# Kernel tuning notes

Hardware: AMD Instinct MI355X
Metric: run time of the kernel (lower is better)

## Reference

```python
import jax, jax.numpy as jnp
import numpy as np

N_NODES = 50000
N_EDGES = 800000
D = 128
N_REL = 4
N_GRAPHS = 128
N_CLASSES = 16


def rgcn_layer(x, W_rel, W_root, b, src, dst, edge_type):
    # Per-relation transform of all nodes: [N, R, D]
    xt = jnp.einsum('nd,rdf->nrf', x, W_rel)
    msg = xt[src, edge_type]  # [E, D] gather message per edge
    # mean aggregation per (dst, relation) pair (PyG RGCNConv aggr='mean')
    seg = dst * N_REL + edge_type
    cnt = jax.ops.segment_sum(jnp.ones((src.shape[0],), x.dtype), seg,
                              num_segments=N_NODES * N_REL)
    norm = 1.0 / jnp.maximum(cnt[seg], 1.0)
    agg = jax.ops.segment_sum(msg * norm[:, None], dst, num_segments=N_NODES)
    return agg + x @ W_root + b


def setup_inputs() -> dict:
    key = jax.random.key(0)
    ks = jax.random.split(key, 12)
    s = 1.0 / np.sqrt(D)
    inp = {
        'x': jax.random.normal(ks[0], (N_NODES, D), jnp.float32),
        'edge_index': jax.random.randint(ks[1], (2, N_EDGES), 0, N_NODES, jnp.int64),
        'edge_type': jax.random.randint(ks[2], (N_EDGES,), 0, N_REL, jnp.int64),
        'batch': jnp.sort(jax.random.randint(ks[3], (N_NODES,), 0, N_GRAPHS, jnp.int64)),
        'W_rel1': jax.random.normal(ks[4], (N_REL, D, D), jnp.float32) * s,
        'W_root1': jax.random.normal(ks[5], (D, D), jnp.float32) * s,
        'b1': jnp.zeros((D,), jnp.float32),
        'W_rel2': jax.random.normal(ks[6], (N_REL, D, D), jnp.float32) * s,
        'W_root2': jax.random.normal(ks[7], (D, D), jnp.float32) * s,
        'b2': jnp.zeros((D,), jnp.float32),
        'W_cls': jax.random.normal(ks[8], (D, N_CLASSES), jnp.float32) * s,
        'b_cls': jnp.zeros((N_CLASSES,), jnp.float32),
    }
    return inp


def reference(x, edge_index, edge_type, batch, W_rel1, W_root1, b1,
              W_rel2, W_root2, b2, W_cls, b_cls):
    src, dst = edge_index[0], edge_index[1]
    h = jax.nn.relu(rgcn_layer(x, W_rel1, W_root1, b1, src, dst, edge_type))
    h = jax.nn.relu(rgcn_layer(h, W_rel2, W_root2, b2, src, dst, edge_type))
    # global mean pool over graphs (dropout is identity: training=False)
    gsum = jax.ops.segment_sum(h, batch, num_segments=N_GRAPHS)
    gcnt = jax.ops.segment_sum(jnp.ones((h.shape[0],), h.dtype), batch,
                               num_segments=N_GRAPHS)
    g = gsum / jnp.maximum(gcnt, 1.0)[:, None]
    return g @ W_cls + b_cls
```

## Files before the change

kernel.cpp:

```cpp
#include <hip/hip_runtime.h>

#define D_DIM 128
#define N_REL 4
#define CAP 32

typedef __attribute__((ext_vector_type(8))) short bf16x8;
typedef __attribute__((ext_vector_type(4))) float f32x4;

static inline int cdiv(int a, int b) { return (a + b - 1) / b; }

__device__ inline ushort f2bf(float f) {
    union { float f; unsigned u; } v;
    v.f = f;
    unsigned r = v.u + 0x7FFFu + ((v.u >> 16) & 1u);
    return (ushort)(r >> 16);
}

__device__ inline float bf2f(ushort u) {
    union { unsigned u; float f; } v;
    v.u = (unsigned)u << 16;
    return v.f;
}

__device__ inline float uif(unsigned u) {
    union { unsigned u; float f; } v;
    v.u = u;
    return v.f;
}

#define CNT_B 391
#define CAST_B 782
#define CAST_FULL 781
#define PACK_B 80

__global__ __launch_bounds__(256) void prep_kernel(
    const float* __restrict__ x, ushort* __restrict__ Xb,
    const int* __restrict__ src, const int* __restrict__ dst,
    const int* __restrict__ et, unsigned* __restrict__ icnt,
    ushort* __restrict__ esorted,
    const float* __restrict__ Wrel1, const float* __restrict__ Wroot1,
    const float* __restrict__ Wrel2, const float* __restrict__ Wroot2,
    ushort* __restrict__ Wpk1, ushort* __restrict__ Wpk2,
    int n4, int nEdges) {
    int b = blockIdx.x;
    if (b < CNT_B) {
        int e = (b * 256 + threadIdx.x) * 8;
        if (e >= nEdges) return;
        if (e + 8 <= nEdges) {
            int4 sA = *(const int4*)(src + e);
            int4 sB = *(const int4*)(src + e + 4);
            int4 dA = *(const int4*)(dst + e);
            int4 dB = *(const int4*)(dst + e + 4);
            int4 tA = *(const int4*)(et + e);
            int4 tB = *(const int4*)(et + e + 4);
            unsigned o0 = atomicAdd(&icnt[dA.x], 1u << (8 * tA.x));
            unsigned o1 = atomicAdd(&icnt[dA.y], 1u << (8 * tA.y));
            unsigned o2 = atomicAdd(&icnt[dA.z], 1u << (8 * tA.z));
            unsigned o3 = atomicAdd(&icnt[dA.w], 1u << (8 * tA.w));
            unsigned o4 = atomicAdd(&icnt[dB.x], 1u << (8 * tB.x));
            unsigned o5 = atomicAdd(&icnt[dB.y], 1u << (8 * tB.y));
            unsigned o6 = atomicAdd(&icnt[dB.z], 1u << (8 * tB.z));
            unsigned o7 = atomicAdd(&icnt[dB.w], 1u << (8 * tB.w));
            int r0 = (int)(((o0 >> (8 * tA.x)) & 0xFFu) - 0xAAu);
            int r1 = (int)(((o1 >> (8 * tA.y)) & 0xFFu) - 0xAAu);
            int r2 = (int)(((o2 >> (8 * tA.z)) & 0xFFu) - 0xAAu);
            int r3 = (int)(((o3 >> (8 * tA.w)) & 0xFFu) - 0xAAu);
            int r4 = (int)(((o4 >> (8 * tB.x)) & 0xFFu) - 0xAAu);
            int r5 = (int)(((o5 >> (8 * tB.y)) & 0xFFu) - 0xAAu);
            int r6 = (int)(((o6 >> (8 * tB.z)) & 0xFFu) - 0xAAu);
            int r7 = (int)(((o7 >> (8 * tB.w)) & 0xFFu) - 0xAAu);
            esorted[((size_t)(dA.x * N_REL + tA.x) << 5) + r0] = (ushort)sA.x;
            esorted[((size_t)(dA.y * N_REL + tA.y) << 5) + r1] = (ushort)sA.y;
            esorted[((size_t)(dA.z * N_REL + tA.z) << 5) + r2] = (ushort)sA.z;
            esorted[((size_t)(dA.w * N_REL + tA.w) << 5) + r3] = (ushort)sA.w;
            esorted[((size_t)(dB.x * N_REL + tB.x) << 5) + r4] = (ushort)sB.x;
            esorted[((size_t)(dB.y * N_REL + tB.y) << 5) + r5] = (ushort)sB.y;
            esorted[((size_t)(dB.z * N_REL + tB.z) << 5) + r6] = (ushort)sB.z;
            esorted[((size_t)(dB.w * N_REL + tB.w) << 5) + r7] = (ushort)sB.w;
        } else {
            for (int j = 0; e + j < nEdges; ++j) {
                int dd = dst[e + j], tt = et[e + j];
                unsigned o = atomicAdd(&icnt[dd], 1u << (8 * tt));
                int r = (int)(((o >> (8 * tt)) & 0xFFu) - 0xAAu);
                esorted[((size_t)(dd * N_REL + tt) << 5) + r] = (ushort)src[e + j];
            }
        }
    } else if (b < CNT_B + CAST_B) {
        int rb = b - CNT_B;
        int base = rb * 2048 + threadIdx.x;
        if (rb < CAST_FULL) {
            float4 v0 = ((const float4*)x)[base];
            float4 v1 = ((const float4*)x)[base + 256];
            float4 v2 = ((const float4*)x)[base + 512];
            float4 v3 = ((const float4*)x)[base + 768];
            float4 v4 = ((const float4*)x)[base + 1024];
            float4 v5 = ((const float4*)x)[base + 1280];
            float4 v6 = ((const float4*)x)[base + 1536];
            float4 v7 = ((const float4*)x)[base + 1792];
            ushort4 o0, o1, o2, o3, o4, o5, o6, o7;
            o0.x = f2bf(v0.x); o0.y = f2bf(v0.y); o0.z = f2bf(v0.z); o0.w = f2bf(v0.w);
            o1.x = f2bf(v1.x); o1.y = f2bf(v1.y); o1.z = f2bf(v1.z); o1.w = f2bf(v1.w);
            o2.x = f2bf(v2.x); o2.y = f2bf(v2.y); o2.z = f2bf(v2.z); o2.w = f2bf(v2.w);
            o3.x = f2bf(v3.x); o3.y = f2bf(v3.y); o3.z = f2bf(v3.z); o3.w = f2bf(v3.w);
            o4.x = f2bf(v4.x); o4.y = f2bf(v4.y); o4.z = f2bf(v4.z); o4.w = f2bf(v4.w);
            o5.x = f2bf(v5.x); o5.y = f2bf(v5.y); o5.z = f2bf(v5.z); o5.w = f2bf(v5.w);
            o6.x = f2bf(v6.x); o6.y = f2bf(v6.y); o6.z = f2bf(v6.z); o6.w = f2bf(v6.w);
            o7.x = f2bf(v7.x); o7.y = f2bf(v7.y); o7.z = f2bf(v7.z); o7.w = f2bf(v7.w);
            ((ushort4*)Xb)[base] = o0;
            ((ushort4*)Xb)[base + 256] = o1;
            ((ushort4*)Xb)[base + 512] = o2;
            ((ushort4*)Xb)[base + 768] = o3;
            ((ushort4*)Xb)[base + 1024] = o4;
            ((ushort4*)Xb)[base + 1280] = o5;
            ((ushort4*)Xb)[base + 1536] = o6;
            ((ushort4*)Xb)[base + 1792] = o7;
        } else {
#pragma unroll
            for (int j = 0; j < 8; ++j) {
                int i = base + j * 256;
                if (i < n4) {
                    float4 v = ((const float4*)x)[i];
                    ushort4 o;
                    o.x = f2bf(v.x); o.y = f2bf(v.y); o.z = f2bf(v.z); o.w = f2bf(v.w);
                    ((ushort4*)Xb)[i] = o;
                }
            }
        }
    } else {
        int pb = b - (CNT_B + CAST_B);
        int layer = pb / 40;
        int rem = pb % 40;
        int mat = rem >> 3;
        int blk = rem & 7;
        const float* Wrel = layer ? Wrel2 : Wrel1;
        const float* Wroot = layer ? Wroot2 : Wroot1;
        ushort* out = layer ? Wpk2 : Wpk1;
        const float* W = (mat < N_REL) ? (Wrel + (size_t)mat * D_DIM * D_DIM) : Wroot;
        int t = blk * 256 + threadIdx.x;
        int lane = t & 63;
        int tile = t >> 6;
        int kt = tile >> 3;
        int nt = tile & 7;
        int n = nt * 16 + (lane & 15);
        int kb = kt * 32 + (lane >> 4) * 8;
        ushort* o = out + (((size_t)mat * 32 + tile) * 64 + lane) * 8;
        ushort4 lo, hi;
        lo.x = f2bf(W[(kb + 0) * D_DIM + n]);
        lo.y = f2bf(W[(kb + 1) * D_DIM + n]);
        lo.z = f2bf(W[(kb + 2) * D_DIM + n]);
        lo.w = f2bf(W[(kb + 3) * D_DIM + n]);
        hi.x = f2bf(W[(kb + 4) * D_DIM + n]);
        hi.y = f2bf(W[(kb + 5) * D_DIM + n]);
        hi.z = f2bf(W[(kb + 6) * D_DIM + n]);
        hi.w = f2bf(W[(kb + 7) * D_DIM + n]);
        *(ushort4*)(o) = lo;
        *(ushort4*)(o + 4) = hi;
    }
}

template <bool DO_SORT>
__global__ __launch_bounds__(256, DO_SORT ? 7 : 8) void layer_kernel(
    const ushort* __restrict__ Xb, const unsigned* __restrict__ icnt,
    ushort* __restrict__ esorted, const ushort* __restrict__ Wpk,
    const float* __restrict__ bias, ushort* __restrict__ outb, int n_nodes) {
    __shared__ ushort Ms[16][520];
    __shared__ ushort sid16[DO_SORT ? 16 : 1][4][34];
    const int tid = threadIdx.x;
    const int wave = tid >> 6;
    const int lane = tid & 63;
    const int ql = tid & 15;
    const int qd = tid >> 4;
    const int m = lane & 15;
    const int q = lane >> 4;
    const int r0 = blockIdx.x * 16;
    const int rel = qd & 3;
    const int rowgrp = qd >> 2;
    const int lanebase = (qd & 3) * 16;

    unsigned cw4[4], idw[4];
#pragma unroll
    for (int p = 0; p < 4; ++p) {
        int node = r0 + p * 4 + rowgrp;
        int vnode = min(node, n_nodes - 1);
        cw4[p] = (node < n_nodes) ? icnt[vnode] : 0xAAAAAAAAu;
        idw[p] = ((const unsigned*)(esorted +
                  (((size_t)vnode * N_REL + rel) << 5)))[ql];
    }

    if constexpr (DO_SORT) {
#pragma unroll
        for (int p = 0; p < 4; ++p) {
            const int deg = (int)(((cw4[p] >> (rel * 8)) & 0xFFu) - 0xAAu);
            if (deg >= 1) {
                const int j0 = 2 * ql, j1 = 2 * ql + 1;
                const int v0 = (int)(idw[p] & 0xFFFFu);
                const int v1 = (int)(idw[p] >> 16);
                int rk0 = 0, rk1 = 0;
                const int nw = (deg + 1) >> 1;
                for (int kk = 0; kk < nw; ++kk) {
                    unsigned w = (unsigned)__shfl((int)idw[p], lanebase + kk, 64);
                    int k0 = 2 * kk, k1 = 2 * kk + 1;
                    int wlo = (int)(w & 0xFFFFu), whi = (int)(w >> 16);
                    rk0 += (wlo < v0 || (wlo == v0 && k0 < j0)) ? 1 : 0;
                    rk1 += (wlo < v1 || (wlo == v1 && k0 < j1)) ? 1 : 0;
                    if (k1 < deg) {
                        rk0 += (whi < v0 || (whi == v0 && k1 < j0)) ? 1 : 0;
                        rk1 += (whi < v1 || (whi == v1 && k1 < j1)) ? 1 : 0;
                    }
                }
                if (j0 < deg) sid16[qd][p][rk0] = (ushort)v0;
                if (j1 < deg) sid16[qd][p][rk1] = (ushort)v1;
            }
        }
        __threadfence_block();
#pragma unroll
        for (int p = 0; p < 4; ++p) {
            const int deg = (int)(((cw4[p] >> (rel * 8)) & 0xFFu) - 0xAAu);
            if (deg >= 2 && 2 * ql < deg) {
                int node = r0 + p * 4 + rowgrp;
                unsigned* rowp = (unsigned*)(esorted +
                                 (((size_t)node * N_REL + rel) << 5));
                rowp[ql] = (unsigned)sid16[qd][p][2 * ql] |
                           ((unsigned)sid16[qd][p][2 * ql + 1] << 16);
            }
        }
        __threadfence_block();
    }

    auto acc8 = [](float* a, uint4 u) {
        a[0] += uif(u.x << 16); a[1] += uif(u.x & 0xFFFF0000u);
        a[2] += uif(u.y << 16); a[3] += uif(u.y & 0xFFFF0000u);
        a[4] += uif(u.z << 16); a[5] += uif(u.z & 0xFFFF0000u);
        a[6] += uif(u.w << 16); a[7] += uif(u.w & 0xFFFF0000u);
    };

    const ushort* xb = Xb + ql * 8;
#pragma unroll
    for (int p = 0; p < 4; ++p) {
        const int row = p * 4 + rowgrp;
        const int deg = (int)(((cw4[p] >> (rel * 8)) & 0xFFu) - 0xAAu);
        uint4* mrow = (uint4*)&Ms[row][rel * 128 + ql * 8];
        if (deg <= 0) {
            *mrow = make_uint4(0u, 0u, 0u, 0u);
            continue;
        }
        auto getid = [&](int e) -> size_t {
            if constexpr (DO_SORT) {
                return (size_t)sid16[qd][p][e] * D_DIM;
            } else {
                unsigned w = (unsigned)__shfl((int)idw[p], lanebase + (e >> 1), 64);
                return (size_t)((e & 1) ? (w >> 16) : (w & 0xFFFFu)) * D_DIM;
            }
        };
        float a[8], b[8];
#pragma unroll
        for (int j = 0; j < 8; ++j) { a[j] = 0.f; b[j] = 0.f; }
        int e = 0;
        for (; e + 4 <= deg; e += 4) {
            size_t s0 = getid(e);
            size_t s1 = getid(e + 1);
            size_t s2 = getid(e + 2);
            size_t s3 = getid(e + 3);
            uint4 u0 = *(const uint4*)(xb + s0);
            uint4 u1 = *(const uint4*)(xb + s1);
            uint4 u2 = *(const uint4*)(xb + s2);
            uint4 u3 = *(const uint4*)(xb + s3);
            acc8(a, u0); acc8(b, u1); acc8(a, u2); acc8(b, u3);
        }
        if (e + 2 <= deg) {
            size_t s0 = getid(e);
            size_t s1 = getid(e + 1);
            uint4 u0 = *(const uint4*)(xb + s0);
            uint4 u1 = *(const uint4*)(xb + s1);
            acc8(a, u0); acc8(b, u1);
            e += 2;
        }
        if (e < deg) {
            uint4 u0 = *(const uint4*)(xb + getid(e));
            acc8(a, u0);
        }
        float sc = 1.0f / (float)deg;
        uint4 o;
        o.x = (unsigned)f2bf((a[0] + b[0]) * sc) | ((unsigned)f2bf((a[1] + b[1]) * sc) << 16);
        o.y = (unsigned)f2bf((a[2] + b[2]) * sc) | ((unsigned)f2bf((a[3] + b[3]) * sc) << 16);
        o.z = (unsigned)f2bf((a[4] + b[4]) * sc) | ((unsigned)f2bf((a[5] + b[5]) * sc) << 16);
        o.w = (unsigned)f2bf((a[6] + b[6]) * sc) | ((unsigned)f2bf((a[7] + b[7]) * sc) << 16);
        *mrow = o;
    }
    __syncthreads();

    f32x4 acc0 = (f32x4){0.f, 0.f, 0.f, 0.f};
    f32x4 acc1 = (f32x4){0.f, 0.f, 0.f, 0.f};
#pragma unroll
    for (int ph = 0; ph < N_REL; ++ph) {
#pragma unroll
        for (int kt = 0; kt < 4; ++kt) {
            bf16x8 a = *(const bf16x8*)&Ms[m][ph * 128 + kt * 32 + q * 8];
            bf16x8 b0 = *(const bf16x8*)(Wpk + (((size_t)ph * 32 + kt * 8 + wave * 2) * 64 + lane) * 8);
            bf16x8 b1 = *(const bf16x8*)(Wpk + (((size_t)ph * 32 + kt * 8 + wave * 2 + 1) * 64 + lane) * 8);
            acc0 = __builtin_amdgcn_mfma_f32_16x16x32_bf16(a, b0, acc0, 0, 0, 0);
            acc1 = __builtin_amdgcn_mfma_f32_16x16x32_bf16(a, b1, acc1, 0, 0, 0);
        }
    }
    {
        const int n0 = min(r0 + m, n_nodes - 1);
        const ushort* aX = Xb + (size_t)n0 * D_DIM + q * 8;
#pragma unroll
        for (int kt = 0; kt < 4; ++kt) {
            bf16x8 a = *(const bf16x8*)(aX + kt * 32);
            bf16x8 b0 = *(const bf16x8*)(Wpk + (((size_t)N_REL * 32 + kt * 8 + wave * 2) * 64 + lane) * 8);
            bf16x8 b1 = *(const bf16x8*)(Wpk + (((size_t)N_REL * 32 + kt * 8 + wave * 2 + 1) * 64 + lane) * 8);
            acc0 = __builtin_amdgcn_mfma_f32_16x16x32_bf16(a, b0, acc0, 0, 0, 0);
            acc1 = __builtin_amdgcn_mfma_f32_16x16x32_bf16(a, b1, acc1, 0, 0, 0);
        }
    }

#pragma unroll
    for (int j = 0; j < 2; ++j) {
        const f32x4 av = j ? acc1 : acc0;
        int col = (wave * 2 + j) * 16 + m;
        float bv = bias[col];
#pragma unroll
        for (int r = 0; r < 4; ++r) {
            int orow = r0 + q * 4 + r;
            if (orow < n_nodes)
                outb[(size_t)orow * D_DIM + col] = f2bf(fmaxf(av[r] + bv, 0.0f));
        }
    }
}

__global__ __launch_bounds__(1024) void poolcls_kernel(
    const ushort* __restrict__ hb, const int* __restrict__ batch,
    const float* __restrict__ Wcls, const float* __restrict__ bcls,
    float* __restrict__ out, int n_nodes) {
    __shared__ float part[64][D_DIM + 1];
    __shared__ float mean[D_DIM];
    __shared__ float cpart[16][17];
    int g = blockIdx.x;
    int tid = threadIdx.x;
    int par = tid >> 4;
    int dg = (tid & 15) * 8;
    auto lb = [&](int val) {
        int lo = 0, hi = n_nodes;
        while (lo < hi) {
            int mid = (lo + hi) >> 1;
            if (batch[mid] < val) lo = mid + 1; else hi = mid;
        }
        return lo;
    };
    int lo = lb(g), hi = lb(g + 1);
    float a[8];
#pragma unroll
    for (int j = 0; j < 8; ++j) a[j] = 0.f;
    for (int nn = lo + par; nn < hi; nn += 64) {
        uint4 u = *(const uint4*)(hb + (size_t)nn * D_DIM + dg);
        a[0] += uif(u.x << 16); a[1] += uif(u.x & 0xFFFF0000u);
        a[2] += uif(u.y << 16); a[3] += uif(u.y & 0xFFFF0000u);
        a[4] += uif(u.z << 16); a[5] += uif(u.z & 0xFFFF0000u);
        a[6] += uif(u.w << 16); a[7] += uif(u.w & 0xFFFF0000u);
    }
#pragma unroll
    for (int j = 0; j < 8; ++j) part[par][dg + j] = a[j];
    __syncthreads();
    if (tid < D_DIM) {
        float s = 0.f;
#pragma unroll
        for (int j = 0; j < 64; ++j) s += part[j][tid];
        mean[tid] = s / fmaxf((float)(hi - lo), 1.0f);
    }
    __syncthreads();
    if (tid < 256) {
        int c = tid & 15, kc = tid >> 4;
        float s = 0.f;
#pragma unroll
        for (int j = 0; j < 8; ++j)
            s = fmaf(mean[kc * 8 + j], Wcls[(kc * 8 + j) * 16 + c], s);
        cpart[kc][c] = s;
    }
    __syncthreads();
    if (tid < 16) {
        float s = bcls[tid];
#pragma unroll
        for (int k = 0; k < 16; ++k) s += cpart[k][tid];
        out[g * 16 + tid] = s;
    }
}

extern "C" void kernel_launch(void* const* d_in, const int* in_sizes, int n_in,
                              void* d_out, int out_size, void* d_ws, size_t ws_size,
                              hipStream_t stream) {
    const float* x      = (const float*)d_in[0];
    const int*   ei     = (const int*)d_in[1];
    const int*   etype  = (const int*)d_in[2];
    const int*   batch  = (const int*)d_in[3];
    const float* Wrel1  = (const float*)d_in[4];
    const float* Wroot1 = (const float*)d_in[5];
    const float* b1     = (const float*)d_in[6];
    const float* Wrel2  = (const float*)d_in[7];
    const float* Wroot2 = (const float*)d_in[8];
    const float* b2     = (const float*)d_in[9];
    const float* Wcls   = (const float*)d_in[10];
    const float* bcls   = (const float*)d_in[11];
    float* out = (float*)d_out;

    const int N = in_sizes[0] / D_DIM;
    const int E = in_sizes[1] / 2;
    const int* src = ei;
    const int* dst = ei + E;

    ushort* Xb   = (ushort*)d_ws;
    ushort* h1b  = Xb + (size_t)N * D_DIM;
    ushort* h2b  = h1b + (size_t)N * D_DIM;
    ushort* Wpk1 = h2b + (size_t)N * D_DIM;
    ushort* Wpk2 = Wpk1 + 81920;
    unsigned* icnt = (unsigned*)(Wpk2 + 81920);
    ushort* esorted = (ushort*)(icnt + N);

    prep_kernel<<<CNT_B + CAST_B + PACK_B, 256, 0, stream>>>(
        x, Xb, src, dst, etype, icnt, esorted, Wrel1, Wroot1, Wrel2, Wroot2,
        Wpk1, Wpk2, N * D_DIM / 4, E);

    layer_kernel<true><<<cdiv(N, 16), 256, 0, stream>>>(
        Xb, icnt, esorted, Wpk1, b1, h1b, N);

    layer_kernel<false><<<cdiv(N, 16), 256, 0, stream>>>(
        h1b, icnt, esorted, Wpk2, b2, h2b, N);

    poolcls_kernel<<<128, 1024, 0, stream>>>(h2b, batch, Wcls, bcls, out, N);
}
```

Baseline: 241.3 us.

## Split layer kernel, halve shared staging in layer 1, use nontemporal prep loads

```diff
diff --git a/kernel.cpp b/kernel.cpp
--- a/kernel.cpp
+++ b/kernel.cpp
@@ -6,6 +6,8 @@
 
 typedef __attribute__((ext_vector_type(8))) short bf16x8;
 typedef __attribute__((ext_vector_type(4))) float f32x4;
+typedef unsigned u32x4 __attribute__((ext_vector_type(4)));
+typedef unsigned u32x2 __attribute__((ext_vector_type(2)));
 
 static inline int cdiv(int a, int b) { return (a + b - 1) / b; }
 
@@ -26,6 +28,23 @@
     union { unsigned u; float f; } v;
     v.u = u;
     return v.f;
+}
+
+__device__ inline int4 ntload_i4(const int* p) {
+    u32x4 v = __builtin_nontemporal_load((const u32x4*)p);
+    return make_int4((int)v.x, (int)v.y, (int)v.z, (int)v.w);
+}
+__device__ inline float4 ntload_f4(const float* p) {
+    u32x4 v = __builtin_nontemporal_load((const u32x4*)p);
+    float4 r;
+    r.x = uif(v.x); r.y = uif(v.y); r.z = uif(v.z); r.w = uif(v.w);
+    return r;
+}
+__device__ inline void ntstore_h4(ushort* p, ushort4 o) {
+    u32x2 v;
+    v.x = (unsigned)o.x | ((unsigned)o.y << 16);
+    v.y = (unsigned)o.z | ((unsigned)o.w << 16);
+    __builtin_nontemporal_store(v, (u32x2*)p);
 }
 
 #define CNT_B 391
@@ -47,12 +66,12 @@
         int e = (b * 256 + threadIdx.x) * 8;
         if (e >= nEdges) return;
         if (e + 8 <= nEdges) {
-            int4 sA = *(const int4*)(src + e);
-            int4 sB = *(const int4*)(src + e + 4);
-            int4 dA = *(const int4*)(dst + e);
-            int4 dB = *(const int4*)(dst + e + 4);
-            int4 tA = *(const int4*)(et + e);
-            int4 tB = *(const int4*)(et + e + 4);
+            int4 sA = ntload_i4(src + e);
+            int4 sB = ntload_i4(src + e + 4);
+            int4 dA = ntload_i4(dst + e);
+            int4 dB = ntload_i4(dst + e + 4);
+            int4 tA = ntload_i4(et + e);
+            int4 tB = ntload_i4(et + e + 4);
             unsigned o0 = atomicAdd(&icnt[dA.x], 1u << (8 * tA.x));
             unsigned o1 = atomicAdd(&icnt[dA.y], 1u << (8 * tA.y));
             unsigned o2 = atomicAdd(&icnt[dA.z], 1u << (8 * tA.z));
@@ -89,14 +108,14 @@
         int rb = b - CNT_B;
         int base = rb * 2048 + threadIdx.x;
         if (rb < CAST_FULL) {
-            float4 v0 = ((const float4*)x)[base];
-            float4 v1 = ((const float4*)x)[base + 256];
-            float4 v2 = ((const float4*)x)[base + 512];
-            float4 v3 = ((const float4*)x)[base + 768];
-            float4 v4 = ((const float4*)x)[base + 1024];
-            float4 v5 = ((const float4*)x)[base + 1280];
-            float4 v6 = ((const float4*)x)[base + 1536];
-            float4 v7 = ((const float4*)x)[base + 1792];
+            float4 v0 = ntload_f4(x + (size_t)base * 4);
+            float4 v1 = ntload_f4(x + (size_t)(base + 256) * 4);
+            float4 v2 = ntload_f4(x + (size_t)(base + 512) * 4);
+            float4 v3 = ntload_f4(x + (size_t)(base + 768) * 4);
+            float4 v4 = ntload_f4(x + (size_t)(base + 1024) * 4);
+            float4 v5 = ntload_f4(x + (size_t)(base + 1280) * 4);
+            float4 v6 = ntload_f4(x + (size_t)(base + 1536) * 4);
+            float4 v7 = ntload_f4(x + (size_t)(base + 1792) * 4);
             ushort4 o0, o1, o2, o3, o4, o5, o6, o7;
             o0.x = f2bf(v0.x); o0.y = f2bf(v0.y); o0.z = f2bf(v0.z); o0.w = f2bf(v0.w);
             o1.x = f2bf(v1.x); o1.y = f2bf(v1.y); o1.z = f2bf(v1.z); o1.w = f2bf(v1.w);
@@ -106,14 +125,14 @@
             o5.x = f2bf(v5.x); o5.y = f2bf(v5.y); o5.z = f2bf(v5.z); o5.w = f2bf(v5.w);
             o6.x = f2bf(v6.x); o6.y = f2bf(v6.y); o6.z = f2bf(v6.z); o6.w = f2bf(v6.w);
             o7.x = f2bf(v7.x); o7.y = f2bf(v7.y); o7.z = f2bf(v7.z); o7.w = f2bf(v7.w);
-            ((ushort4*)Xb)[base] = o0;
-            ((ushort4*)Xb)[base + 256] = o1;
-            ((ushort4*)Xb)[base + 512] = o2;
-            ((ushort4*)Xb)[base + 768] = o3;
-            ((ushort4*)Xb)[base + 1024] = o4;
-            ((ushort4*)Xb)[base + 1280] = o5;
-            ((ushort4*)Xb)[base + 1536] = o6;
-            ((ushort4*)Xb)[base + 1792] = o7;
+            ntstore_h4(Xb + (size_t)base * 4, o0);
+            ntstore_h4(Xb + (size_t)(base + 256) * 4, o1);
+            ntstore_h4(Xb + (size_t)(base + 512) * 4, o2);
+            ntstore_h4(Xb + (size_t)(base + 768) * 4, o3);
+            ntstore_h4(Xb + (size_t)(base + 1024) * 4, o4);
+            ntstore_h4(Xb + (size_t)(base + 1280) * 4, o5);
+            ntstore_h4(Xb + (size_t)(base + 1536) * 4, o6);
+            ntstore_h4(Xb + (size_t)(base + 1792) * 4, o7);
         } else {
 #pragma unroll
             for (int j = 0; j < 8; ++j) {
@@ -158,13 +177,190 @@
     }
 }
 
-template <bool DO_SORT>
-__global__ __launch_bounds__(256, DO_SORT ? 7 : 8) void layer_kernel(
+__device__ inline void acc8fn(float* a, uint4 u) {
+    a[0] += uif(u.x << 16); a[1] += uif(u.x & 0xFFFF0000u);
+    a[2] += uif(u.y << 16); a[3] += uif(u.y & 0xFFFF0000u);
+    a[4] += uif(u.z << 16); a[5] += uif(u.z & 0xFFFF0000u);
+    a[6] += uif(u.w << 16); a[7] += uif(u.w & 0xFFFF0000u);
+}
+
+__global__ __launch_bounds__(256, 8) void layer1_kernel(
     const ushort* __restrict__ Xb, const unsigned* __restrict__ icnt,
     ushort* __restrict__ esorted, const ushort* __restrict__ Wpk,
     const float* __restrict__ bias, ushort* __restrict__ outb, int n_nodes) {
+    __shared__ ushort Ms[16][264];
+    __shared__ ushort sid16[16][4][34];
+    const int tid = threadIdx.x;
+    const int wave = tid >> 6;
+    const int lane = tid & 63;
+    const int ql = tid & 15;
+    const int qd = tid >> 4;
+    const int m = lane & 15;
+    const int q = lane >> 4;
+    const int r0 = blockIdx.x * 16;
+    const int relLo = qd & 1;
+    const int rowgrp = qd >> 1;
+    const int lanebase = (qd & 3) * 16;
+
+    unsigned cw2[2], idw[2][2];
+#pragma unroll
+    for (int p = 0; p < 2; ++p) {
+        int node = r0 + p * 8 + rowgrp;
+        int vnode = min(node, n_nodes - 1);
+        cw2[p] = (node < n_nodes) ? icnt[vnode] : 0xAAAAAAAAu;
+#pragma unroll
+        for (int P = 0; P < 2; ++P) {
+            idw[P][p] = ((const unsigned*)(esorted +
+                         (((size_t)vnode * N_REL + 2 * P + relLo) << 5)))[ql];
+        }
+    }
+
+#pragma unroll
+    for (int P = 0; P < 2; ++P) {
+#pragma unroll
+        for (int p = 0; p < 2; ++p) {
+            const int rel = 2 * P + relLo;
+            const int deg = (int)(((cw2[p] >> (rel * 8)) & 0xFFu) - 0xAAu);
+            if (deg >= 1) {
+                const int j0 = 2 * ql, j1 = 2 * ql + 1;
+                const int v0 = (int)(idw[P][p] & 0xFFFFu);
+                const int v1 = (int)(idw[P][p] >> 16);
+                int rk0 = 0, rk1 = 0;
+                const int nw = (deg + 1) >> 1;
+                for (int kk = 0; kk < nw; ++kk) {
+                    unsigned w = (unsigned)__shfl((int)idw[P][p], lanebase + kk, 64);
+                    int k0 = 2 * kk, k1 = 2 * kk + 1;
+                    int wlo = (int)(w & 0xFFFFu), whi = (int)(w >> 16);
+                    rk0 += (wlo < v0 || (wlo == v0 && k0 < j0)) ? 1 : 0;
+                    rk1 += (wlo < v1 || (wlo == v1 && k0 < j1)) ? 1 : 0;
+                    if (k1 < deg) {
+                        rk0 += (whi < v0 || (whi == v0 && k1 < j0)) ? 1 : 0;
+                        rk1 += (whi < v1 || (whi == v1 && k1 < j1)) ? 1 : 0;
+                    }
+                }
+                if (j0 < deg) sid16[qd][P * 2 + p][rk0] = (ushort)v0;
+                if (j1 < deg) sid16[qd][P * 2 + p][rk1] = (ushort)v1;
+            }
+        }
+    }
+    __threadfence_block();
+#pragma unroll
+    for (int P = 0; P < 2; ++P) {
+#pragma unroll
+        for (int p = 0; p < 2; ++p) {
+            const int rel = 2 * P + relLo;
+            const int deg = (int)(((cw2[p] >> (rel * 8)) & 0xFFu) - 0xAAu);
+            if (deg >= 2 && 2 * ql < deg) {
+                int node = r0 + p * 8 + rowgrp;
+                unsigned* rowp = (unsigned*)(esorted +
+                                 (((size_t)node * N_REL + rel) << 5));
+                rowp[ql] = (unsigned)sid16[qd][P * 2 + p][2 * ql] |
+                           ((unsigned)sid16[qd][P * 2 + p][2 * ql + 1] << 16);
+            }
+        }
+    }
+    __threadfence_block();
+
+    f32x4 acc0 = (f32x4){0.f, 0.f, 0.f, 0.f};
+    f32x4 acc1 = (f32x4){0.f, 0.f, 0.f, 0.f};
+    const ushort* xb = Xb + ql * 8;
+
+#pragma unroll
+    for (int P = 0; P < 2; ++P) {
+#pragma unroll
+        for (int p = 0; p < 2; ++p) {
+            const int row = p * 8 + rowgrp;
+            const int rel = 2 * P + relLo;
+            const int deg = (int)(((cw2[p] >> (rel * 8)) & 0xFFu) - 0xAAu);
+            uint4* mrow = (uint4*)&Ms[row][relLo * 128 + ql * 8];
+            if (deg <= 0) {
+                *mrow = make_uint4(0u, 0u, 0u, 0u);
+                continue;
+            }
+            const ushort* sp = sid16[qd][P * 2 + p];
+            float a[8], bb[8];
+#pragma unroll
+            for (int j = 0; j < 8; ++j) { a[j] = 0.f; bb[j] = 0.f; }
+            int e = 0;
+            for (; e + 4 <= deg; e += 4) {
+                size_t s0 = (size_t)sp[e] * D_DIM;
+                size_t s1 = (size_t)sp[e + 1] * D_DIM;
+                size_t s2 = (size_t)sp[e + 2] * D_DIM;
+                size_t s3 = (size_t)sp[e + 3] * D_DIM;
+                uint4 u0 = *(const uint4*)(xb + s0);
+                uint4 u1 = *(const uint4*)(xb + s1);
+                uint4 u2 = *(const uint4*)(xb + s2);
+                uint4 u3 = *(const uint4*)(xb + s3);
+                acc8fn(a, u0); acc8fn(bb, u1); acc8fn(a, u2); acc8fn(bb, u3);
+            }
+            if (e + 2 <= deg) {
+                size_t s0 = (size_t)sp[e] * D_DIM;
+                size_t s1 = (size_t)sp[e + 1] * D_DIM;
+                uint4 u0 = *(const uint4*)(xb + s0);
+                uint4 u1 = *(const uint4*)(xb + s1);
+                acc8fn(a, u0); acc8fn(bb, u1);
+                e += 2;
+            }
+            if (e < deg) {
+                uint4 u0 = *(const uint4*)(xb + (size_t)sp[e] * D_DIM);
+                acc8fn(a, u0);
+            }
+            float sc = 1.0f / (float)deg;
+            uint4 o;
+            o.x = (unsigned)f2bf((a[0] + bb[0]) * sc) | ((unsigned)f2bf((a[1] + bb[1]) * sc) << 16);
+            o.y = (unsigned)f2bf((a[2] + bb[2]) * sc) | ((unsigned)f2bf((a[3] + bb[3]) * sc) << 16);
+            o.z = (unsigned)f2bf((a[4] + bb[4]) * sc) | ((unsigned)f2bf((a[5] + bb[5]) * sc) << 16);
+            o.w = (unsigned)f2bf((a[6] + bb[6]) * sc) | ((unsigned)f2bf((a[7] + bb[7]) * sc) << 16);
+            *mrow = o;
+        }
+        __syncthreads();
+#pragma unroll
+        for (int phl = 0; phl < 2; ++phl) {
+            const int ph = 2 * P + phl;
+#pragma unroll
+            for (int kt = 0; kt < 4; ++kt) {
+                bf16x8 a = *(const bf16x8*)&Ms[m][phl * 128 + kt * 32 + q * 8];
+                bf16x8 b0 = *(const bf16x8*)(Wpk + (((size_t)ph * 32 + kt * 8 + wave * 2) * 64 + lane) * 8);
+                bf16x8 b1 = *(const bf16x8*)(Wpk + (((size_t)ph * 32 + kt * 8 + wave * 2 + 1) * 64 + lane) * 8);
+                acc0 = __builtin_amdgcn_mfma_f32_16x16x32_bf16(a, b0, acc0, 0, 0, 0);
+                acc1 = __builtin_amdgcn_mfma_f32_16x16x32_bf16(a, b1, acc1, 0, 0, 0);
+            }
+        }
+        if (P == 0) __syncthreads();
+    }
+
+    {
+        const int n0 = min(r0 + m, n_nodes - 1);
+        const ushort* aX = Xb + (size_t)n0 * D_DIM + q * 8;
+#pragma unroll
+        for (int kt = 0; kt < 4; ++kt) {
+            bf16x8 a = *(const bf16x8*)(aX + kt * 32);
+            bf16x8 b0 = *(const bf16x8*)(Wpk + (((size_t)N_REL * 32 + kt * 8 + wave * 2) * 64 + lane) * 8);
+            bf16x8 b1 = *(const bf16x8*)(Wpk + (((size_t)N_REL * 32 + kt * 8 + wave * 2 + 1) * 64 + lane) * 8);
+            acc0 = __builtin_amdgcn_mfma_f32_16x16x32_bf16(a, b0, acc0, 0, 0, 0);
+            acc1 = __builtin_amdgcn_mfma_f32_16x16x32_bf16(a, b1, acc1, 0, 0, 0);
+        }
+    }
+
+#pragma unroll
+    for (int j = 0; j < 2; ++j) {
+        const f32x4 av = j ? acc1 : acc0;
+        int col = (wave * 2 + j) * 16 + m;
+        float bv = bias[col];
+#pragma unroll
+        for (int r = 0; r < 4; ++r) {
+            int orow = r0 + q * 4 + r;
+            if (orow < n_nodes)
+                outb[(size_t)orow * D_DIM + col] = f2bf(fmaxf(av[r] + bv, 0.0f));
+        }
+    }
+}
+
+__global__ __launch_bounds__(256, 8) void layer2_kernel(
+    const ushort* __restrict__ Xb, const unsigned* __restrict__ icnt,
+    const ushort* __restrict__ esorted, const ushort* __restrict__ Wpk,
+    const float* __restrict__ bias, ushort* __restrict__ outb, int n_nodes) {
     __shared__ ushort Ms[16][520];
-    __shared__ ushort sid16[DO_SORT ? 16 : 1][4][34];
     const int tid = threadIdx.x;
     const int wave = tid >> 6;
     const int lane = tid & 63;
@@ -187,53 +383,6 @@
                   (((size_t)vnode * N_REL + rel) << 5)))[ql];
     }
 
-    if constexpr (DO_SORT) {
-#pragma unroll
-        for (int p = 0; p < 4; ++p) {
-            const int deg = (int)(((cw4[p] >> (rel * 8)) & 0xFFu) - 0xAAu);
-            if (deg >= 1) {
-                const int j0 = 2 * ql, j1 = 2 * ql + 1;
-                const int v0 = (int)(idw[p] & 0xFFFFu);
-                const int v1 = (int)(idw[p] >> 16);
-                int rk0 = 0, rk1 = 0;
-                const int nw = (deg + 1) >> 1;
-                for (int kk = 0; kk < nw; ++kk) {
-                    unsigned w = (unsigned)__shfl((int)idw[p], lanebase + kk, 64);
-                    int k0 = 2 * kk, k1 = 2 * kk + 1;
-                    int wlo = (int)(w & 0xFFFFu), whi = (int)(w >> 16);
-                    rk0 += (wlo < v0 || (wlo == v0 && k0 < j0)) ? 1 : 0;
-                    rk1 += (wlo < v1 || (wlo == v1 && k0 < j1)) ? 1 : 0;
-                    if (k1 < deg) {
-                        rk0 += (whi < v0 || (whi == v0 && k1 < j0)) ? 1 : 0;
-                        rk1 += (whi < v1 || (whi == v1 && k1 < j1)) ? 1 : 0;
-                    }
-                }
-                if (j0 < deg) sid16[qd][p][rk0] = (ushort)v0;
-                if (j1 < deg) sid16[qd][p][rk1] = (ushort)v1;
-            }
-        }
-        __threadfence_block();
-#pragma unroll
-        for (int p = 0; p < 4; ++p) {
-            const int deg = (int)(((cw4[p] >> (rel * 8)) & 0xFFu) - 0xAAu);
-            if (deg >= 2 && 2 * ql < deg) {
-                int node = r0 + p * 4 + rowgrp;
-                unsigned* rowp = (unsigned*)(esorted +
-                                 (((size_t)node * N_REL + rel) << 5));
-                rowp[ql] = (unsigned)sid16[qd][p][2 * ql] |
-                           ((unsigned)sid16[qd][p][2 * ql + 1] << 16);
-            }
-        }
-        __threadfence_block();
-    }
-
-    auto acc8 = [](float* a, uint4 u) {
-        a[0] += uif(u.x << 16); a[1] += uif(u.x & 0xFFFF0000u);
-        a[2] += uif(u.y << 16); a[3] += uif(u.y & 0xFFFF0000u);
-        a[4] += uif(u.z << 16); a[5] += uif(u.z & 0xFFFF0000u);
-        a[6] += uif(u.w << 16); a[7] += uif(u.w & 0xFFFF0000u);
-    };
-
     const ushort* xb = Xb + ql * 8;
 #pragma unroll
     for (int p = 0; p < 4; ++p) {
@@ -245,16 +394,12 @@
             continue;
         }
         auto getid = [&](int e) -> size_t {
-            if constexpr (DO_SORT) {
-                return (size_t)sid16[qd][p][e] * D_DIM;
-            } else {
-                unsigned w = (unsigned)__shfl((int)idw[p], lanebase + (e >> 1), 64);
-                return (size_t)((e & 1) ? (w >> 16) : (w & 0xFFFFu)) * D_DIM;
-            }
+            unsigned w = (unsigned)__shfl((int)idw[p], lanebase + (e >> 1), 64);
+            return (size_t)((e & 1) ? (w >> 16) : (w & 0xFFFFu)) * D_DIM;
         };
-        float a[8], b[8];
-#pragma unroll
-        for (int j = 0; j < 8; ++j) { a[j] = 0.f; b[j] = 0.f; }
+        float a[8], bb[8];
+#pragma unroll
+        for (int j = 0; j < 8; ++j) { a[j] = 0.f; bb[j] = 0.f; }
         int e = 0;
         for (; e + 4 <= deg; e += 4) {
             size_t s0 = getid(e);
@@ -265,26 +410,26 @@
             uint4 u1 = *(const uint4*)(xb + s1);
             uint4 u2 = *(const uint4*)(xb + s2);
             uint4 u3 = *(const uint4*)(xb + s3);
-            acc8(a, u0); acc8(b, u1); acc8(a, u2); acc8(b, u3);
+            acc8fn(a, u0); acc8fn(bb, u1); acc8fn(a, u2); acc8fn(bb, u3);
         }
         if (e + 2 <= deg) {
             size_t s0 = getid(e);
             size_t s1 = getid(e + 1);
             uint4 u0 = *(const uint4*)(xb + s0);
             uint4 u1 = *(const uint4*)(xb + s1);
-            acc8(a, u0); acc8(b, u1);
+            acc8fn(a, u0); acc8fn(bb, u1);
             e += 2;
         }
         if (e < deg) {
             uint4 u0 = *(const uint4*)(xb + getid(e));
-            acc8(a, u0);
+            acc8fn(a, u0);
         }
         float sc = 1.0f / (float)deg;
         uint4 o;
-        o.x = (unsigned)f2bf((a[0] + b[0]) * sc) | ((unsigned)f2bf((a[1] + b[1]) * sc) << 16);
-        o.y = (unsigned)f2bf((a[2] + b[2]) * sc) | ((unsigned)f2bf((a[3] + b[3]) * sc) << 16);
-        o.z = (unsigned)f2bf((a[4] + b[4]) * sc) | ((unsigned)f2bf((a[5] + b[5]) * sc) << 16);
-        o.w = (unsigned)f2bf((a[6] + b[6]) * sc) | ((unsigned)f2bf((a[7] + b[7]) * sc) << 16);
+        o.x = (unsigned)f2bf((a[0] + bb[0]) * sc) | ((unsigned)f2bf((a[1] + bb[1]) * sc) << 16);
+        o.y = (unsigned)f2bf((a[2] + bb[2]) * sc) | ((unsigned)f2bf((a[3] + bb[3]) * sc) << 16);
+        o.z = (unsigned)f2bf((a[4] + bb[4]) * sc) | ((unsigned)f2bf((a[5] + bb[5]) * sc) << 16);
+        o.w = (unsigned)f2bf((a[6] + bb[6]) * sc) | ((unsigned)f2bf((a[7] + bb[7]) * sc) << 16);
         *mrow = o;
     }
     __syncthreads();
@@ -420,10 +565,10 @@
         x, Xb, src, dst, etype, icnt, esorted, Wrel1, Wroot1, Wrel2, Wroot2,
         Wpk1, Wpk2, N * D_DIM / 4, E);
 
-    layer_kernel<true><<<cdiv(N, 16), 256, 0, stream>>>(
+    layer1_kernel<<<cdiv(N, 16), 256, 0, stream>>>(
         Xb, icnt, esorted, Wpk1, b1, h1b, N);
 
-    layer_kernel<false><<<cdiv(N, 16), 256, 0, stream>>>(
+    layer2_kernel<<<cdiv(N, 16), 256, 0, stream>>>(
         h1b, icnt, esorted, Wpk2, b2, h2b, N);
 
     poolcls_kernel<<<128, 1024, 0, stream>>>(h2b, batch, Wcls, bcls, out, N);
```

Result: slower. 256.1 us (+6.1%).
